# Performance work log

Hardware: AMD Instinct MI355X
Metric: run time of the kernel (lower is better)

## Reference

```python
import jax, jax.numpy as jnp
import numpy as np

# Module hyperparameters (from init_kwargs)
P = 96                 # num_of_patches
W = 1536.0             # input width
H = 1536.0             # input height
XPS = W / P            # x patch size = 16
YPS = H / P            # y patch size = 16
PROB_THR = 0.9
IOU_THR = 0.5
N = P * P              # total candidate boxes


def setup_inputs() -> dict:
    key = jax.random.key(0)
    # x: [5, P, P] -> channel 0 = probability, 1..4 = (x, y, w, h) in [0,1)
    x = jax.random.uniform(key, (5, P, P), dtype=jnp.float32)
    return {"x": x}


def _pairwise_iou(b):
    # b: [N, 4] xyxy
    x1, y1, x2, y2 = b[:, 0], b[:, 1], b[:, 2], b[:, 3]
    area = (x2 - x1) * (y2 - y1)                       # [N]
    ix1 = jnp.maximum(x1[:, None], x1[None, :])
    iy1 = jnp.maximum(y1[:, None], y1[None, :])
    ix2 = jnp.minimum(x2[:, None], x2[None, :])
    iy2 = jnp.minimum(y2[:, None], y2[None, :])
    inter = jnp.clip(ix2 - ix1, 0.0) * jnp.clip(iy2 - iy1, 0.0)
    union = area[:, None] + area[None, :] - inter
    return jnp.where(union > 0, inter / union, 0.0)    # [N, N]


def _forward(x):
    # --- scale_batch_bbx_xywh, applied densely (invalid entries are masked later) ---
    p = x[0]
    ii = jnp.arange(P, dtype=x.dtype)[:, None]   # row index i
    jj = jnp.arange(P, dtype=x.dtype)[None, :]   # col index j
    bx = x[1] * XPS + ii * XPS
    by = x[2] * YPS + jj * YPS
    bw = x[3] * W
    bh = x[4] * H
    bbx = jnp.stack([p, bx, by, bw, bh], axis=0).reshape(5, N).T   # [N, 5] (p, x, y, w, h)

    # --- remove_low_probability_bbx: fixed-shape validity mask instead of filtering ---
    scores = bbx[:, 0]
    valid = scores > PROB_THR

    # --- convert_batch_to_xyxy + round ---
    x1 = jnp.round(bbx[:, 1])
    y1 = jnp.round(bbx[:, 2])
    x2 = jnp.round(bbx[:, 3] + bbx[:, 1])
    y2 = jnp.round(bbx[:, 4] + bbx[:, 2])

    # --- greedy NMS (torchvision semantics): sort by score desc, suppress by IoU ---
    sort_key = jnp.where(valid, scores, -jnp.inf)
    order = jnp.argsort(-sort_key)
    boxes = jnp.stack([x1, y1, x2, y2], axis=1)[order]   # [N, 4] sorted
    sc = scores[order]
    v = valid[order]
    iou = _pairwise_iou(boxes)                           # [N, N]

    def body(kept, i):
        suppressed = jnp.any(kept & (iou[i] > IOU_THR))
        ki = v[i] & ~suppressed
        return kept.at[i].set(ki), ki

    _, keeps = jax.lax.scan(body, jnp.zeros((N,), bool), jnp.arange(N))

    # --- cat([scores, bbx]) then convert_batch_to_xywh on kept rows ---
    out = jnp.stack(
        [sc, boxes[:, 0], boxes[:, 1], boxes[:, 2] - boxes[:, 0], boxes[:, 3] - boxes[:, 1]],
        axis=1,
    )  # [N, 5] = (score, x, y, w, h), score-descending order like nms output
    out = jnp.where(keeps[:, None], out, 0.0)
    return out, keeps


def reference(x):
    # Returns (out [N,5], keep_mask [N]); rows with keep_mask=False are zeroed.
    # This is the fixed-shape equivalent of the variable-length torch output.
    return _forward(x)
```

## Files before the change

### kernel.cpp

```cpp
#include <hip/hip_runtime.h>

#define PP 96
#define NB (PP*PP)
#define NCH (NB/64)
#define PROB_THR 0.9f
#define FAST_CAP 1024
#define LSTRIDE 1034
#define NPROD 32
#define PTHR 512

typedef unsigned long long u64;
typedef unsigned int u32;

__device__ __forceinline__ void decode_box(const float* __restrict__ x, int n,
                                           float& X1, float& Y1, float& X2, float& Y2)
{
    float xv = x[NB + n];
    float yv = x[2 * NB + n];
    float wv = x[3 * NB + n];
    float hv = x[4 * NB + n];
    int i = n / PP;
    int j = n - i * PP;
    float bx = __fadd_rn(__fmul_rn(xv, 16.0f), (float)i * 16.0f);
    float by = __fadd_rn(__fmul_rn(yv, 16.0f), (float)j * 16.0f);
    float bw = __fmul_rn(wv, 1536.0f);
    float bh = __fmul_rn(hv, 1536.0f);
    X1 = rintf(bx);
    Y1 = rintf(by);
    X2 = rintf(__fadd_rn(bw, bx));
    Y2 = rintf(__fadd_rn(bh, by));
}

__device__ __forceinline__ int iou_hit_nodiv(float ix1, float iy1, float ix2, float iy2, float iar,
                                             float jx1, float jy1, float jx2, float jy2, float jar)
{
    float xx1 = fmaxf(ix1, jx1), yy1 = fmaxf(iy1, jy1);
    float xx2 = fminf(ix2, jx2), yy2 = fminf(iy2, jy2);
    float iw = fmaxf(__fsub_rn(xx2, xx1), 0.0f);
    float ih = fmaxf(__fsub_rn(yy2, yy1), 0.0f);
    float inter = __fmul_rn(iw, ih);
    float uni = __fsub_rn(__fadd_rn(iar, jar), inter);
    return (uni > 0.0f && __fadd_rn(inter, inter) > uni) ? 1 : 0;
}

__device__ __forceinline__ int iou_hit_div(float ix1, float iy1, float ix2, float iy2, float iar,
                                           float jx1, float jy1, float jx2, float jy2, float jar)
{
    float xx1 = fmaxf(ix1, jx1), yy1 = fmaxf(iy1, jy1);
    float xx2 = fminf(ix2, jx2), yy2 = fminf(iy2, jy2);
    float iw = fmaxf(__fsub_rn(xx2, xx1), 0.0f);
    float ih = fmaxf(__fsub_rn(yy2, yy1), 0.0f);
    float inter = __fmul_rn(iw, ih);
    float uni = __fsub_rn(__fadd_rn(iar, jar), inter);
    return (uni > 0.0f && __fdiv_rn(inter, uni) > 0.5f) ? 1 : 0;
}

__global__ void __launch_bounds__(PTHR) k_prepadj(
    const float* __restrict__ x, float* __restrict__ out,
    float* __restrict__ gss,
    float* __restrict__ gx1, float* __restrict__ gy1,
    float* __restrict__ gx2, float* __restrict__ gy2,
    u64* __restrict__ skeys, int* __restrict__ counter,
    u64* __restrict__ adjT, long long cap_words)
{
    __shared__ u64 lmask[NCH];
    __shared__ int pc[NCH], loff[NCH];
    __shared__ int sM;
    __shared__ u64 kdb[FAST_CAP];
    __shared__ float bx1[FAST_CAP], by1[FAST_CAP], bx2[FAST_CAP], by2[FAST_CAP], bss[FAST_CAP];

    const int tid = threadIdx.x;
    const int lane = tid & 63;
    const int wv = tid >> 6;
    const int b = blockIdx.x;

    for (int q = tid; q < 432; q += PTHR)
        ((float4*)out)[b * 432 + q] = make_float4(0.f, 0.f, 0.f, 0.f);

    for (int c = wv; c < NCH; c += 8) {
        float s = x[(c << 6) + lane];
        u64 m = __ballot(s > PROB_THR);
        if (lane == 0) lmask[c] = m;
    }
    __syncthreads();
    if (tid < NCH) pc[tid] = __popcll(lmask[tid]);
    __syncthreads();
    if (tid < 64) {
        int acc = 0;
        for (int seg = 0; seg < 3; ++seg) {
            int c = (seg << 6) + lane;
            int pv = (c < NCH) ? pc[c] : 0;
            int v = pv;
            #pragma unroll
            for (int off = 1; off < 64; off <<= 1) {
                int u = __shfl_up(v, off);
                if (lane >= off) v += u;
            }
            if (c < NCH) loff[c] = acc + v - pv;
            acc += __shfl(v, 63);
        }
        if (lane == 0) sM = acc;
    }
    __syncthreads();
    const int M = sM;
    const int W = (M + 63) >> 6;
    const bool fast = (M <= FAST_CAP) && (cap_words >= 16384);

    if (b == 0 && tid == 0) counter[0] = M;

    if (!fast) {
        if (b == 0) {
            for (int c = wv; c < NCH; c += 8) {
                float s = x[(c << 6) + lane];
                u64 m = lmask[c];
                if ((m >> lane) & 1ull) {
                    int pos = loff[c] + __popcll(m & ((1ull << lane) - 1ull));
                    int n = (c << 6) + lane;
                    skeys[pos] = ((u64)__float_as_uint(s) << 32) | (u64)(NB - 1 - n);
                }
            }
        }
        return;
    }
    if ((b << 5) >= M) return;

    for (int c = wv; c < NCH; c += 8) {
        float s = x[(c << 6) + lane];
        u64 m = lmask[c];
        if ((m >> lane) & 1ull) {
            int pos = loff[c] + __popcll(m & ((1ull << lane) - 1ull));
            int n = (c << 6) + lane;
            kdb[pos] = ((u64)__float_as_uint(s) << 32) | (u64)(NB - 1 - n);
        }
    }
    int S = 64; while (S < M) S <<= 1;
    for (int q = M + tid; q < S; q += PTHR) kdb[q] = 0ull;
    __syncthreads();
    for (int k = 2; k <= S; k <<= 1) {
        for (int j = k >> 1; j > 0; j >>= 1) {
            for (int p = tid; p < S; p += PTHR) {
                int q2 = p ^ j;
                if (q2 > p) {
                    u64 a = kdb[p], c2 = kdb[q2];
                    if ((a < c2) == ((p & k) == 0)) { kdb[p] = c2; kdb[q2] = a; }
                }
            }
            __syncthreads();
        }
    }
    for (int r = tid; r < M; r += PTHR) {
        u64 key = kdb[r];
        int n = NB - 1 - (int)(key & 0xFFFFFFFFull);
        float X1, Y1, X2, Y2;
        decode_box(x, n, X1, Y1, X2, Y2);
        bx1[r] = X1; by1[r] = Y1; bx2[r] = X2; by2[r] = Y2;
        bss[r] = __uint_as_float((unsigned)(key >> 32));
    }
    __syncthreads();

    if (b == 0) {
        for (int r = tid; r < M; r += PTHR) {
            gss[r] = bss[r];
            gx1[r] = bx1[r]; gy1[r] = by1[r];
            gx2[r] = bx2[r]; gy2[r] = by2[r];
        }
    }

    for (int ri = 0; ri < 4; ++ri) {
        int i = (b << 5) + (ri << 3) + wv;
        if (i >= M) break;
        float ix1 = bx1[i], iy1 = by1[i], ix2 = bx2[i], iy2 = by2[i];
        float iar = __fmul_rn(__fsub_rn(ix2, ix1), __fsub_rn(iy2, iy1));
        for (int kk = 0; kk < W; ++kk) {
            int j = (kk << 6) + lane;
            float jx1 = bx1[j & (FAST_CAP-1)], jy1 = by1[j & (FAST_CAP-1)];
            float jx2 = bx2[j & (FAST_CAP-1)], jy2 = by2[j & (FAST_CAP-1)];
            float jar = __fmul_rn(__fsub_rn(jx2, jx1), __fsub_rn(jy2, jy1));
            int hit = (j < M) && iou_hit_nodiv(ix1, iy1, ix2, iy2, iar,
                                               jx1, jy1, jx2, jy2, jar);
            u64 mm = __ballot(hit);
            if (lane == 0) adjT[(size_t)kk * 1024 + i] = mm;
        }
    }
}

#define SUBCHUNK(DSRC)                                                        \
    {                                                                         \
        const ulonglong2* cp2 = (const ulonglong2*)(Lds + cbase + (sc << 3)); \
        const ulonglong2* rp2 = (const ulonglong2*)(Lds + rbase + (sc << 3)); \
        ulonglong2 ca = cp2[0], cb = cp2[1], cc = cp2[2], cd = cp2[3];        \
        ulonglong2 ra = rp2[0], rbv = rp2[1], rc = rp2[2], rd = rp2[3];       \
        u64 colb[8] = {ca.x, ca.y, cb.x, cb.y, cc.x, cc.y, cd.x, cd.y};       \
        u64 rowb[8] = {ra.x, ra.y, rbv.x, rbv.y, rc.x, rc.y, rd.x, rd.y};     \
        _Pragma("unroll")                                                     \
        for (int t = 0; t < 8; ++t) {                                         \
            const int bitp = (sc << 3) + t;                                   \
            u32 bbit = ((DSRC) >> bitp) & 1u;                                 \
            u32 m = bbit - 1u;                     \
            dl |= (u32)colb[t] & m;                                           \
            dh |= (u32)(colb[t] >> 32) & m;                                   \
            supl |= (u32)rowb[t] & m;                                         \
            suph |= (u32)(rowb[t] >> 32) & m;                                 \
            kw |= m & (1u << bitp);                                           \
        }                                                                     \
    }

__global__ void __launch_bounds__(256) k_sweep(
    const float* __restrict__ x, float* __restrict__ out,
    float* __restrict__ gss,
    float* __restrict__ gx1, float* __restrict__ gy1,
    float* __restrict__ gx2, float* __restrict__ gy2,
    const u64* __restrict__ skeys, const int* __restrict__ counter,
    const u64* __restrict__ adjT, long long cap_words)
{
    __shared__ __align__(16) u64 Lds[16 * LSTRIDE];
    __shared__ u64 keepw[NCH];
    int M = counter[0]; if (M > NB) M = NB;
    const int W = (M + 63) >> 6;
    const bool fast = (M <= FAST_CAP) && (cap_words >= 16384);
    const int tid = threadIdx.x, lane = tid & 63;

    if (fast) {
        const int npair = W << 9;
        const ulonglong2* gp = (const ulonglong2*)adjT;
        for (int f = tid; f < npair; f += 256) {
            int w = f >> 9, r2 = f & 511;
            ((ulonglong2*)Lds)[w * (LSTRIDE >> 1) + r2] = gp[f];
        }
        __syncthreads();

        if (tid < 64) {
            const int wl = (lane < W) ? lane : 0;
            u32 supl = 0u, suph = 0u, dl = 0u, dh = 0u;
            u64 mykw = 0ull;
            const int nrb = (M + 31) >> 5;
            for (int rb = 0; rb < nrb; ++rb) {
                const int c = rb >> 1;
                const int base = rb << 5;
                const size_t cbase = (size_t)c * LSTRIDE + base;
                const size_t rbase = (size_t)wl * LSTRIDE + base;
                if (!(rb & 1)) {
                    if (rb == 0) { dl = 0u; dh = 0u; }
                    else { dl = (u32)__shfl((int)supl, c); dh = (u32)__shfl((int)suph, c); }
                    int rem = M - (c << 6);
                    if (rem < 64) {
                        if (rem >= 32) dh |= 0xFFFFFFFFu << (rem - 32);
                        else { dh = 0xFFFFFFFFu; dl |= 0xFFFFFFFFu << rem; }
                    }
                }
                u32 kw = 0u;
                if (!(rb & 1)) {
                    #pragma unroll
                    for (int sc = 0; sc < 4; ++sc) SUBCHUNK(dl)
                } else {
                    #pragma unroll
                    for (int sc = 0; sc < 4; ++sc) SUBCHUNK(dh)
                }
                mykw |= (lane == c) ? ((u64)kw << ((rb & 1) << 5)) : 0ull;
            }
            keepw[lane] = mykw;
        }
    } else {
        for (int t = tid; t < M; t += 256) {
            u64 key = skeys[t];
            int r = 0;
            for (int q = 0; q < M; ++q) r += (skeys[q] > key) ? 1 : 0;
            int n = NB - 1 - (int)(key & 0xFFFFFFFFull);
            float X1, Y1, X2, Y2;
            decode_box(x, n, X1, Y1, X2, Y2);
            gss[r] = __uint_as_float((unsigned)(key >> 32));
            gx1[r] = X1; gy1[r] = Y1; gx2[r] = X2; gy2[r] = Y2;
        }
        __threadfence_block();
        __syncthreads();
        if (tid < 64) {
            u64 kbs[3] = {0ull, 0ull, 0ull};
            for (int i = 0; i < M; ++i) {
                float ix1 = gx1[i], iy1 = gy1[i], ix2 = gx2[i], iy2 = gy2[i];
                float iar = __fmul_rn(__fsub_rn(ix2, ix1), __fsub_rn(iy2, iy1));
                int hit = 0;
                int nk = (i > lane) ? ((i - lane + 63) >> 6) : 0;
                for (int w = 0; w < 3 && !hit; ++w) {
                    int klim = nk - (w << 6);
                    if (klim <= 0) break;
                    u64 bits = kbs[w];
                    if (klim < 64) bits &= ((1ull << klim) - 1ull);
                    while (bits) {
                        int kk2 = __builtin_ctzll(bits);
                        bits &= bits - 1ull;
                        int jj = lane + (((w << 6) + kk2) << 6);
                        float jx1 = gx1[jj], jy1 = gy1[jj], jx2 = gx2[jj], jy2 = gy2[jj];
                        float jar = __fmul_rn(__fsub_rn(jx2, jx1), __fsub_rn(jy2, jy1));
                        if (iou_hit_div(ix1, iy1, ix2, iy2, iar, jx1, jy1, jx2, jy2, jar)) { hit = 1; break; }
                    }
                }
                int suppressed = __any(hit);
                if (!suppressed && lane == (i & 63)) kbs[(i >> 6) >> 6] |= 1ull << ((i >> 6) & 63);
            }
            int NWrd = (M + 63) >> 6;
            for (int wd = 0; wd < NWrd; ++wd) {
                u64 bit = (kbs[wd >> 6] >> (wd & 63)) & 1ull;
                u64 word = __ballot(bit != 0);
                if (lane == 0 && wd < NCH) keepw[wd] = word;
            }
        }
    }
    __syncthreads();

    for (int i = tid; i < M; i += 256) {
        if ((keepw[i >> 6] >> (i & 63)) & 1ull) {
            float a = gx1[i], b2 = gy1[i], c2 = gx2[i], d = gy2[i];
            out[i * 5 + 0] = gss[i];
            out[i * 5 + 1] = a;
            out[i * 5 + 2] = b2;
            out[i * 5 + 3] = __fsub_rn(c2, a);
            out[i * 5 + 4] = __fsub_rn(d, b2);
            out[5 * NB + i] = 1.0f;
        }
    }
}

extern "C" void kernel_launch(void* const* d_in, const int* in_sizes, int n_in,
                              void* d_out, int out_size, void* d_ws, size_t ws_size,
                              hipStream_t stream) {
    const float* x = (const float*)d_in[0];
    float* out = (float*)d_out;

    char* ws = (char*)d_ws;
    int* counter = (int*)ws;
    float* fb  = (float*)(ws + 16);
    float* gss = fb + 0 * NB;
    float* gx1 = fb + 1 * NB;
    float* gy1 = fb + 2 * NB;
    float* gx2 = fb + 3 * NB;
    float* gy2 = fb + 4 * NB;
    size_t adj_off = 16 + (size_t)5 * NB * 4;
    u64* adjT  = (u64*)(ws + adj_off);
    u64* skeys = adjT;
    long long cap_words = (ws_size > adj_off) ? (long long)((ws_size - adj_off) / 8) : 0;

    k_prepadj<<<NPROD, PTHR, 0, stream>>>(x, out, gss, gx1, gy1, gx2, gy2,
                                          skeys, counter, adjT, cap_words);
    k_sweep<<<1, 256, 0, stream>>>(x, out, gss, gx1, gy1, gx2, gy2,
                                   skeys, counter, adjT, cap_words);
}
```

Measured before the change: 126.0 us.

## Split sort and adjacency into separate kernels with rank-count sort

Replaces the single prep kernel, in which 32 blocks each redundantly ran the same bitonic sort, with one sort kernel that ranks the keys by counting, using readlane broadcast. That sort kernel writes boxes as float4 to global memory. A 64-block adjacency kernel then loads the sorted boxes and builds the IoU bitmask, and the sweep kernel batches its loads of the adjacency matrix into LDS. The goal is to remove the redundant per-block sort and the many barrier-bound bitonic stages, at the cost of an extra kernel launch and a trip through global memory between stages.

```diff
diff --git a/kernel.cpp b/kernel.cpp
--- a/kernel.cpp
+++ b/kernel.cpp
@@ -6,19 +6,13 @@
 #define PROB_THR 0.9f
 #define FAST_CAP 1024
 #define LSTRIDE 1034
-#define NPROD 32
-#define PTHR 512
 
 typedef unsigned long long u64;
 typedef unsigned int u32;
 
-__device__ __forceinline__ void decode_box(const float* __restrict__ x, int n,
-                                           float& X1, float& Y1, float& X2, float& Y2)
-{
-    float xv = x[NB + n];
-    float yv = x[2 * NB + n];
-    float wv = x[3 * NB + n];
-    float hv = x[4 * NB + n];
+__device__ __forceinline__ void decode_core(int n, float xv, float yv, float wv, float hv,
+                                            float& X1, float& Y1, float& X2, float& Y2)
+{
     int i = n / PP;
     int j = n - i * PP;
     float bx = __fadd_rn(__fmul_rn(xv, 16.0f), (float)i * 16.0f);
@@ -31,6 +25,12 @@
     Y2 = rintf(__fadd_rn(bh, by));
 }
 
+__device__ __forceinline__ void decode_box(const float* __restrict__ x, int n,
+                                           float& X1, float& Y1, float& X2, float& Y2)
+{
+    decode_core(n, x[NB + n], x[2 * NB + n], x[3 * NB + n], x[4 * NB + n], X1, Y1, X2, Y2);
+}
+
 __device__ __forceinline__ int iou_hit_nodiv(float ix1, float iy1, float ix2, float iy2, float iar,
                                              float jx1, float jy1, float jx2, float jy2, float jar)
 {
@@ -55,32 +55,31 @@
     return (uni > 0.0f && __fdiv_rn(inter, uni) > 0.5f) ? 1 : 0;
 }
 
-__global__ void __launch_bounds__(PTHR) k_prepadj(
-    const float* __restrict__ x, float* __restrict__ out,
-    float* __restrict__ gss,
-    float* __restrict__ gx1, float* __restrict__ gy1,
-    float* __restrict__ gx2, float* __restrict__ gy2,
-    u64* __restrict__ skeys, int* __restrict__ counter,
-    u64* __restrict__ adjT, long long cap_words)
+__global__ void __launch_bounds__(512) k_sort(
+    const float* __restrict__ x,
+    float* __restrict__ gss, float4* __restrict__ gbox,
+    u64* __restrict__ skeys, int* __restrict__ counter, int ws_ok)
 {
     __shared__ u64 lmask[NCH];
     __shared__ int pc[NCH], loff[NCH];
     __shared__ int sM;
     __shared__ u64 kdb[FAST_CAP];
-    __shared__ float bx1[FAST_CAP], by1[FAST_CAP], bx2[FAST_CAP], by2[FAST_CAP], bss[FAST_CAP];
 
     const int tid = threadIdx.x;
     const int lane = tid & 63;
     const int wv = tid >> 6;
-    const int b = blockIdx.x;
-
-    for (int q = tid; q < 432; q += PTHR)
-        ((float4*)out)[b * 432 + q] = make_float4(0.f, 0.f, 0.f, 0.f);
-
-    for (int c = wv; c < NCH; c += 8) {
-        float s = x[(c << 6) + lane];
-        u64 m = __ballot(s > PROB_THR);
-        if (lane == 0) lmask[c] = m;
+
+    #pragma unroll
+    for (int g = 0; g < 18; g += 6) {
+        float sv[6];
+        #pragma unroll
+        for (int u = 0; u < 6; ++u)
+            sv[u] = x[((wv + ((g + u) << 3)) << 6) + lane];
+        #pragma unroll
+        for (int u = 0; u < 6; ++u) {
+            u64 m = __ballot(sv[u] > PROB_THR);
+            if (lane == 0) lmask[wv + ((g + u) << 3)] = m;
+        }
     }
     __syncthreads();
     if (tid < NCH) pc[tid] = __popcll(lmask[tid]);
@@ -103,26 +102,21 @@
     }
     __syncthreads();
     const int M = sM;
-    const int W = (M + 63) >> 6;
-    const bool fast = (M <= FAST_CAP) && (cap_words >= 16384);
-
-    if (b == 0 && tid == 0) counter[0] = M;
+    const bool fast = (M <= FAST_CAP) && ws_ok;
+    if (tid == 0) counter[0] = M;
 
     if (!fast) {
-        if (b == 0) {
-            for (int c = wv; c < NCH; c += 8) {
-                float s = x[(c << 6) + lane];
-                u64 m = lmask[c];
-                if ((m >> lane) & 1ull) {
-                    int pos = loff[c] + __popcll(m & ((1ull << lane) - 1ull));
-                    int n = (c << 6) + lane;
-                    skeys[pos] = ((u64)__float_as_uint(s) << 32) | (u64)(NB - 1 - n);
-                }
+        for (int c = wv; c < NCH; c += 8) {
+            float s = x[(c << 6) + lane];
+            u64 m = lmask[c];
+            if ((m >> lane) & 1ull) {
+                int pos = loff[c] + __popcll(m & ((1ull << lane) - 1ull));
+                int n = (c << 6) + lane;
+                skeys[pos] = ((u64)__float_as_uint(s) << 32) | (u64)(NB - 1 - n);
             }
         }
         return;
     }
-    if ((b << 5) >= M) return;
 
     for (int c = wv; c < NCH; c += 8) {
         float s = x[(c << 6) + lane];
@@ -133,53 +127,81 @@
             kdb[pos] = ((u64)__float_as_uint(s) << 32) | (u64)(NB - 1 - n);
         }
     }
-    int S = 64; while (S < M) S <<= 1;
-    for (int q = M + tid; q < S; q += PTHR) kdb[q] = 0ull;
-    __syncthreads();
-    for (int k = 2; k <= S; k <<= 1) {
-        for (int j = k >> 1; j > 0; j >>= 1) {
-            for (int p = tid; p < S; p += PTHR) {
-                int q2 = p ^ j;
-                if (q2 > p) {
-                    u64 a = kdb[p], c2 = kdb[q2];
-                    if ((a < c2) == ((p & k) == 0)) { kdb[p] = c2; kdb[q2] = a; }
-                }
-            }
-            __syncthreads();
-        }
-    }
-    for (int r = tid; r < M; r += PTHR) {
-        u64 key = kdb[r];
-        int n = NB - 1 - (int)(key & 0xFFFFFFFFull);
+    for (int q = M + tid; q < FAST_CAP; q += 512) kdb[q] = 0ull;
+    __syncthreads();
+
+    u64 k0 = kdb[tid], k1 = kdb[tid + 512];
+    int n0 = NB - 1 - (int)(k0 & 0xFFFFFFFFull);
+    int n1 = NB - 1 - (int)(k1 & 0xFFFFFFFFull);
+    float xv0 = x[NB + n0], yv0 = x[2 * NB + n0], wv0 = x[3 * NB + n0], hv0 = x[4 * NB + n0];
+    float xv1 = x[NB + n1], yv1 = x[2 * NB + n1], wv1 = x[3 * NB + n1], hv1 = x[4 * NB + n1];
+    int r0 = 0, r1 = 0;
+    const int nck = (M + 63) >> 6;
+    for (int ch = 0; ch < nck; ++ch) {
+        u64 kq = kdb[(ch << 6) + lane];
+        u32 qlo = (u32)kq, qhi = (u32)(kq >> 32);
+        #pragma unroll
+        for (int i = 0; i < 64; ++i) {
+            u32 blo = (u32)__builtin_amdgcn_readlane((int)qlo, i);
+            u32 bhi = (u32)__builtin_amdgcn_readlane((int)qhi, i);
+            u64 kb = ((u64)bhi << 32) | (u64)blo;
+            r0 += (kb > k0) ? 1 : 0;
+            r1 += (kb > k1) ? 1 : 0;
+        }
+    }
+    if (tid < M) {
         float X1, Y1, X2, Y2;
-        decode_box(x, n, X1, Y1, X2, Y2);
-        bx1[r] = X1; by1[r] = Y1; bx2[r] = X2; by2[r] = Y2;
-        bss[r] = __uint_as_float((unsigned)(key >> 32));
-    }
-    __syncthreads();
-
-    if (b == 0) {
-        for (int r = tid; r < M; r += PTHR) {
-            gss[r] = bss[r];
-            gx1[r] = bx1[r]; gy1[r] = by1[r];
-            gx2[r] = bx2[r]; gy2[r] = by2[r];
-        }
-    }
-
-    for (int ri = 0; ri < 4; ++ri) {
-        int i = (b << 5) + (ri << 3) + wv;
+        decode_core(n0, xv0, yv0, wv0, hv0, X1, Y1, X2, Y2);
+        gbox[r0] = make_float4(X1, Y1, X2, Y2);
+        gss[r0] = __uint_as_float((u32)(k0 >> 32));
+    }
+    if (tid + 512 < M) {
+        float X1, Y1, X2, Y2;
+        decode_core(n1, xv1, yv1, wv1, hv1, X1, Y1, X2, Y2);
+        gbox[r1] = make_float4(X1, Y1, X2, Y2);
+        gss[r1] = __uint_as_float((u32)(k1 >> 32));
+    }
+}
+
+__global__ void __launch_bounds__(256) k_adj(
+    float* __restrict__ out, const float4* __restrict__ gbox,
+    const int* __restrict__ counter, u64* __restrict__ adjT, int ws_ok)
+{
+    __shared__ float4 lb[FAST_CAP];
+    __shared__ float la[FAST_CAP];
+    int M = counter[0]; if (M > NB) M = NB;
+    const int tid = threadIdx.x, lane = tid & 63, wv = tid >> 6, b = blockIdx.x;
+
+    float4 z4 = make_float4(0.f, 0.f, 0.f, 0.f);
+    for (int q = tid; q < 216; q += 256)
+        ((float4*)out)[b * 216 + q] = z4;
+
+    const bool fast = (M <= FAST_CAP) && ws_ok;
+    if (!fast) return;
+    if ((b << 4) >= M) return;
+
+    const int W = (M + 63) >> 6;
+    for (int f = tid; f < M; f += 256) {
+        float4 bb = gbox[f];
+        lb[f] = bb;
+        la[f] = __fmul_rn(__fsub_rn(bb.z, bb.x), __fsub_rn(bb.w, bb.y));
+    }
+    __syncthreads();
+
+    #pragma unroll
+    for (int r = 0; r < 4; ++r) {
+        int i = (b << 4) + (r << 2) + wv;
         if (i >= M) break;
-        float ix1 = bx1[i], iy1 = by1[i], ix2 = bx2[i], iy2 = by2[i];
-        float iar = __fmul_rn(__fsub_rn(ix2, ix1), __fsub_rn(iy2, iy1));
+        float4 bi = lb[i];
+        float iar = la[i];
         for (int kk = 0; kk < W; ++kk) {
             int j = (kk << 6) + lane;
-            float jx1 = bx1[j & (FAST_CAP-1)], jy1 = by1[j & (FAST_CAP-1)];
-            float jx2 = bx2[j & (FAST_CAP-1)], jy2 = by2[j & (FAST_CAP-1)];
-            float jar = __fmul_rn(__fsub_rn(jx2, jx1), __fsub_rn(jy2, jy1));
-            int hit = (j < M) && iou_hit_nodiv(ix1, iy1, ix2, iy2, iar,
-                                               jx1, jy1, jx2, jy2, jar);
+            float4 bj = lb[j & (FAST_CAP - 1)];
+            float jar = la[j & (FAST_CAP - 1)];
+            int hit = (j < M) && iou_hit_nodiv(bi.x, bi.y, bi.z, bi.w, iar,
+                                               bj.x, bj.y, bj.z, bj.w, jar);
             u64 mm = __ballot(hit);
-            if (lane == 0) adjT[(size_t)kk * 1024 + i] = mm;
+            if (lane == 0) adjT[((size_t)kk << 10) + i] = mm;
         }
     }
 }
@@ -207,25 +229,36 @@
 
 __global__ void __launch_bounds__(256) k_sweep(
     const float* __restrict__ x, float* __restrict__ out,
-    float* __restrict__ gss,
-    float* __restrict__ gx1, float* __restrict__ gy1,
-    float* __restrict__ gx2, float* __restrict__ gy2,
+    float* __restrict__ gss, float4* __restrict__ gbox,
     const u64* __restrict__ skeys, const int* __restrict__ counter,
-    const u64* __restrict__ adjT, long long cap_words)
+    const u64* __restrict__ adjT, int ws_ok)
 {
     __shared__ __align__(16) u64 Lds[16 * LSTRIDE];
     __shared__ u64 keepw[NCH];
     int M = counter[0]; if (M > NB) M = NB;
     const int W = (M + 63) >> 6;
-    const bool fast = (M <= FAST_CAP) && (cap_words >= 16384);
+    const bool fast = (M <= FAST_CAP) && ws_ok;
     const int tid = threadIdx.x, lane = tid & 63;
 
     if (fast) {
         const int npair = W << 9;
         const ulonglong2* gp = (const ulonglong2*)adjT;
-        for (int f = tid; f < npair; f += 256) {
-            int w = f >> 9, r2 = f & 511;
-            ((ulonglong2*)Lds)[w * (LSTRIDE >> 1) + r2] = gp[f];
+        for (int r = 0; r < 4; ++r) {
+            int fb = (r << 11) + tid;
+            ulonglong2 v[8];
+            #pragma unroll
+            for (int u = 0; u < 8; ++u) {
+                int f = fb + (u << 8);
+                v[u] = (f < npair) ? gp[f] : make_ulonglong2(0ull, 0ull);
+            }
+            #pragma unroll
+            for (int u = 0; u < 8; ++u) {
+                int f = fb + (u << 8);
+                if (f < npair) {
+                    int w = f >> 9, r2 = f & 511;
+                    ((ulonglong2*)Lds)[w * (LSTRIDE >> 1) + r2] = v[u];
+                }
+            }
         }
         __syncthreads();
 
@@ -268,16 +301,16 @@
             int n = NB - 1 - (int)(key & 0xFFFFFFFFull);
             float X1, Y1, X2, Y2;
             decode_box(x, n, X1, Y1, X2, Y2);
-            gss[r] = __uint_as_float((unsigned)(key >> 32));
-            gx1[r] = X1; gy1[r] = Y1; gx2[r] = X2; gy2[r] = Y2;
-        }
-        __threadfence_block();
+            gbox[r] = make_float4(X1, Y1, X2, Y2);
+            gss[r] = __uint_as_float((u32)(key >> 32));
+        }
+        __threadfence();
         __syncthreads();
         if (tid < 64) {
             u64 kbs[3] = {0ull, 0ull, 0ull};
             for (int i = 0; i < M; ++i) {
-                float ix1 = gx1[i], iy1 = gy1[i], ix2 = gx2[i], iy2 = gy2[i];
-                float iar = __fmul_rn(__fsub_rn(ix2, ix1), __fsub_rn(iy2, iy1));
+                float4 bi = gbox[i];
+                float iar = __fmul_rn(__fsub_rn(bi.z, bi.x), __fsub_rn(bi.w, bi.y));
                 int hit = 0;
                 int nk = (i > lane) ? ((i - lane + 63) >> 6) : 0;
                 for (int w = 0; w < 3 && !hit; ++w) {
@@ -289,9 +322,10 @@
                         int kk2 = __builtin_ctzll(bits);
                         bits &= bits - 1ull;
                         int jj = lane + (((w << 6) + kk2) << 6);
-                        float jx1 = gx1[jj], jy1 = gy1[jj], jx2 = gx2[jj], jy2 = gy2[jj];
-                        float jar = __fmul_rn(__fsub_rn(jx2, jx1), __fsub_rn(jy2, jy1));
-                        if (iou_hit_div(ix1, iy1, ix2, iy2, iar, jx1, jy1, jx2, jy2, jar)) { hit = 1; break; }
+                        float4 bj = gbox[jj];
+                        float jar = __fmul_rn(__fsub_rn(bj.z, bj.x), __fsub_rn(bj.w, bj.y));
+                        if (iou_hit_div(bi.x, bi.y, bi.z, bi.w, iar,
+                                        bj.x, bj.y, bj.z, bj.w, jar)) { hit = 1; break; }
                     }
                 }
                 int suppressed = __any(hit);
@@ -309,12 +343,12 @@
 
     for (int i = tid; i < M; i += 256) {
         if ((keepw[i >> 6] >> (i & 63)) & 1ull) {
-            float a = gx1[i], b2 = gy1[i], c2 = gx2[i], d = gy2[i];
+            float4 bb = gbox[i];
             out[i * 5 + 0] = gss[i];
-            out[i * 5 + 1] = a;
-            out[i * 5 + 2] = b2;
-            out[i * 5 + 3] = __fsub_rn(c2, a);
-            out[i * 5 + 4] = __fsub_rn(d, b2);
+            out[i * 5 + 1] = bb.x;
+            out[i * 5 + 2] = bb.y;
+            out[i * 5 + 3] = __fsub_rn(bb.z, bb.x);
+            out[i * 5 + 4] = __fsub_rn(bb.w, bb.y);
             out[5 * NB + i] = 1.0f;
         }
     }
@@ -328,19 +362,15 @@
 
     char* ws = (char*)d_ws;
     int* counter = (int*)ws;
-    float* fb  = (float*)(ws + 16);
-    float* gss = fb + 0 * NB;
-    float* gx1 = fb + 1 * NB;
-    float* gy1 = fb + 2 * NB;
-    float* gx2 = fb + 3 * NB;
-    float* gy2 = fb + 4 * NB;
-    size_t adj_off = 16 + (size_t)5 * NB * 4;
-    u64* adjT  = (u64*)(ws + adj_off);
-    u64* skeys = adjT;
-    long long cap_words = (ws_size > adj_off) ? (long long)((ws_size - adj_off) / 8) : 0;
-
-    k_prepadj<<<NPROD, PTHR, 0, stream>>>(x, out, gss, gx1, gy1, gx2, gy2,
-                                          skeys, counter, adjT, cap_words);
-    k_sweep<<<1, 256, 0, stream>>>(x, out, gss, gx1, gy1, gx2, gy2,
-                                   skeys, counter, adjT, cap_words);
-}
+    float*  gss  = (float*)(ws + 16);
+    float4* gbox = (float4*)(ws + 16 + (size_t)4 * NB);
+    u64*    adjT = (u64*)(ws + 16 + (size_t)4 * NB + (size_t)16 * NB);
+    u64*    skeys = (u64*)((char*)adjT + (size_t)16384 * 8);
+    const size_t NEEDED = 16 + (size_t)4 * NB + (size_t)16 * NB
+                        + (size_t)16384 * 8 + (size_t)8 * NB;
+    int ws_ok = (ws_size >= NEEDED) ? 1 : 0;
+
+    k_sort<<<1, 512, 0, stream>>>(x, gss, gbox, skeys, counter, ws_ok);
+    k_adj<<<64, 256, 0, stream>>>(out, gbox, counter, adjT, ws_ok);
+    k_sweep<<<1, 256, 0, stream>>>(x, out, gss, gbox, skeys, counter, adjT, ws_ok);
+}
```

New measurement: 119.0 us. 1.06x faster.
